# Kernel tuning notes

Hardware: AMD Instinct MI355X
Metric: run time of the kernel (lower is better)

The kernel has to match this reference:

```python
import jax, jax.numpy as jnp
import numpy as np

D_OUT = 32


def mlp(x, Ws, bs):
    # Ws: (L+1, d, d), bs: (L+1, d); relu after hidden layers, linear output
    h = x
    n = Ws.shape[0]
    for i in range(n - 1):
        h = jax.nn.relu(h @ Ws[i] + bs[i])
    return h @ Ws[n - 1] + bs[n - 1]


def causal_dot_product(Q, K, V, t1, t2):
    """out[:,:,i] = Q_i @ sum_{j: t2[j] <= t1[i]} K_j V_j^T.
    t2 is sorted (timestamps), so the cumulative outer-product state can be
    computed with a cumsum and gathered via searchsorted.
    Q: (1,1,T1,d); K,V: (1,1,T2,d); t1: (T1,); t2: (T2,).
    """
    outer = K[..., :, :, None] * V[..., :, None, :]      # (1,1,T2,d,d)
    S = jnp.cumsum(outer, axis=2)                        # prefix states
    idx = jnp.searchsorted(t2, t1, side='right') - 1     # (T1,)
    valid = idx >= 0
    Sg = S[:, :, jnp.maximum(idx, 0)]                    # (1,1,T1,d,d)
    out = jnp.einsum('bhid,bhide->bhie', Q, Sg)
    return jnp.where(valid[None, None, :, None], out, jnp.zeros((), out.dtype))


def _with_sorted_time(x, key):
    T = x.shape[2]
    t = jnp.sort(jax.random.uniform(key, (T,), dtype=jnp.float32)) * 100.0
    return x.at[0, 0, :, -1].set(t)


def setup_inputs() -> dict:
    key = jax.random.key(0)
    ks = jax.random.split(key, 16)
    d = 64
    Ts = [4096, 6144, 8192, 4096]
    mods = {}
    for i, T in enumerate(Ts):
        x = jax.random.normal(ks[i], (1, 1, T, d), dtype=jnp.float32)
        mods[f'm{i+1}'] = _with_sorted_time(x, ks[8 + i])
    scale = 1.0 / np.sqrt(d)
    WQ_w = jax.random.normal(ks[4], (3, d, d), dtype=jnp.float32) * scale
    WQ_b = jnp.zeros((3, d), dtype=jnp.float32)
    WK_w = jax.random.normal(ks[5], (4, 3, d, d), dtype=jnp.float32) * scale
    WK_b = jnp.zeros((4, 3, d), dtype=jnp.float32)
    return dict(m1=mods['m1'], m2=mods['m2'], m3=mods['m3'], m4=mods['m4'],
                WQ_w=WQ_w, WQ_b=WQ_b, WK_w=WK_w, WK_b=WK_b)


def reference(m1, m2, m3, m4, WQ_w, WQ_b, WK_w, WK_b):
    Q = mlp(m1, WQ_w, WQ_b)            # (1,1,T1,d)
    t1 = m1[0, 0, :, -1]               # (T1,)
    total = None
    for mi, X in enumerate([m1, m2, m3, m4]):
        K = mlp(X, WK_w[mi], WK_b[mi])
        V = X
        t2 = X[0, 0, :, -1]
        Z = causal_dot_product(Q, K, V, t1, t2)  # (1,1,T1,d)
        total = Z if total is None else total + Z
    # cat over dim=1 then sum(1) == sum of per-modality results, dim 1 dropped
    yhat = total.sum(axis=1)[..., :D_OUT]        # (1,T1,d_out)
    return yhat
```

## Files before the change

kernel.cpp:

```cpp
#include <hip/hip_runtime.h>


#define QB_OFF   0
#define KB_OFF   131072
#define SP_OFF   851968
#define TD_OFF   1581056

typedef __attribute__((ext_vector_type(8))) short short8;
typedef __attribute__((ext_vector_type(4))) float floatx4;

__device__ __forceinline__ unsigned short f2bf(float f) {
    union { float f; unsigned u; } v; v.f = f;
    unsigned r = v.u + 0x7fff + ((v.u >> 16) & 1);
    return (unsigned short)(r >> 16);
}
__device__ __forceinline__ float bf2f(unsigned short h) {
    union { unsigned u; float f; } v; v.u = ((unsigned)h) << 16;
    return v.f;
}

#define MFMA16(a,b,c) __builtin_amdgcn_mfma_f32_16x16x32_bf16((a),(b),(c),0,0,0)

__global__ __launch_bounds__(256) void k_fused(
    const float* __restrict__ x0, const float* __restrict__ x1,
    const float* __restrict__ x2, const float* __restrict__ x3,
    const float* __restrict__ wq_w, const float* __restrict__ wq_b,
    const float* __restrict__ wk_w, const float* __restrict__ wk_b,
    float* __restrict__ ws, float* __restrict__ out)
{
    __shared__ unsigned short H0[64*72];
    __shared__ unsigned short H1[64*72];
    __shared__ unsigned short Wt[3][64*72];
    __shared__ unsigned short KT[64*72];
    __shared__ unsigned short VT[32*72];

    const int tid = threadIdx.x;
    const int bid = blockIdx.x;

    int task, rb;
    if (bid < 64)       { task = 0; rb = bid; }
    else if (bid < 128) { task = 1; rb = bid - 64; }
    else if (bid < 224) { task = 2; rb = bid - 128; }
    else if (bid < 352) { task = 3; rb = bid - 224; }
    else                { task = 4; rb = bid - 352; }

    const float* Xs[4] = {x0, x1, x2, x3};
    const int rowoff[4] = {0, 4096, 10240, 18432};
    const int spoffc[4] = {0, 64, 160, 288};

    const float* X; const float* W; const float* Bv; int mm = -1;
    if (task == 0) { X = x0; W = wq_w; Bv = wq_b; }
    else {
        mm = task - 1;
        X = Xs[mm]; W = wk_w + mm*3*64*64; Bv = wk_b + mm*3*64;
    }

    const int row0 = rb * 64;

    {
        const float4* X4 = (const float4*)(X + (size_t)row0*64);
        #pragma unroll
        for (int k = 0; k < 4; ++k) {
            int idx = k*256 + tid;
            float4 v = X4[idx];
            int rr = idx >> 4, c4 = (idx & 15) * 4;
            ushort4 h;
            h.x = f2bf(v.x); h.y = f2bf(v.y); h.z = f2bf(v.z); h.w = f2bf(v.w);
            *(ushort4*)&H0[rr*72 + c4] = h;
        }
        const float4* W4 = (const float4*)W;
        #pragma unroll
        for (int k = 0; k < 12; ++k) {
            int idx = k*256 + tid;
            float4 v = W4[idx];
            int l = idx >> 10, rest = idx & 1023;
            int d = rest >> 4, c4 = (rest & 15) * 4;
            Wt[l][(c4+0)*72 + d] = f2bf(v.x);
            Wt[l][(c4+1)*72 + d] = f2bf(v.y);
            Wt[l][(c4+2)*72 + d] = f2bf(v.z);
            Wt[l][(c4+3)*72 + d] = f2bf(v.w);
        }
    }
    if (task == 0) {
        float4 z = make_float4(0.f, 0.f, 0.f, 0.f);
        ((float4*)out)[bid*512 + tid] = z;
        ((float4*)out)[bid*512 + 256 + tid] = z;
    }
    if (task > 0 && tid < 64)
        ws[TD_OFF + rowoff[mm] + row0 + tid] = X[(size_t)(row0 + tid)*64 + 63];
    __syncthreads();

    const int w    = tid >> 6;
    const int lane = tid & 63;
    const int lm   = lane & 15;
    const int q    = lane >> 4;
    const int col  = w*16 + lm;

    #pragma unroll 1
    for (int l = 0; l < 3; ++l) {
        const unsigned short* Hin  = (l & 1) ? H1 : H0;
        unsigned short*       Hout = (l & 1) ? H0 : H1;
        float bias = Bv[l*64 + col];
        short8 b0 = *(const short8*)&Wt[l][col*72 + q*8];
        short8 b1 = *(const short8*)&Wt[l][col*72 + 32 + q*8];
        #pragma unroll
        for (int mt = 0; mt < 4; ++mt) {
            floatx4 acc = {bias, bias, bias, bias};
            short8 a0 = *(const short8*)&Hin[(mt*16+lm)*72 + q*8];
            short8 a1 = *(const short8*)&Hin[(mt*16+lm)*72 + 32 + q*8];
            acc = MFMA16(a0, b0, acc);
            acc = MFMA16(a1, b1, acc);
            int r0 = mt*16 + q*4;
            #pragma unroll
            for (int r = 0; r < 4; ++r) {
                float f = acc[r];
                if (l < 2) f = fmaxf(f, 0.0f);
                unsigned short hb = f2bf(f);
                Hout[(r0+r)*72 + col] = hb;
                if (l == 2 && task > 0) KT[col*72 + r0 + r] = hb;
            }
        }
        __syncthreads();
    }

    {
        unsigned short* dst = (task == 0)
            ? (unsigned short*)(ws + QB_OFF)
            : (unsigned short*)(ws + KB_OFF) + (size_t)rowoff[mm]*64;
        #pragma unroll
        for (int k = 0; k < 4; ++k) {
            int idx = k*256 + tid;
            int rr = idx >> 4, c4 = (idx & 15) * 4;
            *(ushort4*)&dst[(size_t)(row0 + rr)*64 + c4] = *(ushort4*)&H1[rr*72 + c4];
        }
    }
    if (task == 0) return;

    {
        #pragma unroll
        for (int k = 0; k < 2; ++k) {
            int idx = k*256 + tid;
            int j = idx >> 3, e4 = (idx & 7) * 4;
            float4 v = *(const float4*)&X[(size_t)(row0 + j)*64 + e4];
            VT[(e4+0)*72 + j] = f2bf(v.x);
            VT[(e4+1)*72 + j] = f2bf(v.y);
            VT[(e4+2)*72 + j] = f2bf(v.z);
            VT[(e4+3)*72 + j] = f2bf(v.w);
        }
    }
    __syncthreads();

    {
        unsigned short* slotH = (unsigned short*)(ws + SP_OFF)
                              + (size_t)(spoffc[mm] + rb) * 2048;
        #pragma unroll
        for (int nt = 0; nt < 2; ++nt) {
            floatx4 acc = {0.f, 0.f, 0.f, 0.f};
            #pragma unroll
            for (int ks = 0; ks < 2; ++ks) {
                short8 aa = *(const short8*)&KT[col*72 + ks*32 + q*8];
                short8 bb = *(const short8*)&VT[(nt*16+lm)*72 + ks*32 + q*8];
                acc = MFMA16(aa, bb, acc);
            }
            #pragma unroll
            for (int r = 0; r < 4; ++r)
                slotH[(w*16 + q*4 + r)*32 + nt*16 + lm] = f2bf(acc[r]);
        }
    }
}

__global__ __launch_bounds__(256) void k_query(
    const float* __restrict__ x0, const float* __restrict__ x1,
    const float* __restrict__ x2, const float* __restrict__ x3,
    float* __restrict__ ws, float* __restrict__ out)
{
    __shared__ unsigned short qs[64*72];
    __shared__ unsigned short kc[64*72];
    __shared__ unsigned short vt[32*72];
    __shared__ unsigned short st[32*72];
    __shared__ unsigned short ps[64*72];
    __shared__ float tq[64];
    __shared__ float tcs[64];
    __shared__ int   SB[2];

    const int tid  = threadIdx.x;
    const int m    = blockIdx.x & 3;
    const int tile = (blockIdx.x >> 2) & 63;
    const int slot = blockIdx.x >> 8;
    const int i0   = tile * 64;

    const int w    = tid >> 6;
    const int lane = tid & 63;
    const int lm   = lane & 15;
    const int q    = lane >> 4;

    const float* Xs[4] = {x0, x1, x2, x3};
    const int rowoff[4] = {0, 4096, 10240, 18432};
    const int spoffc[4] = {0, 64, 160, 288};
    const int Tm[4]     = {4096, 6144, 8192, 4096};
    const float* X = Xs[m];

    const unsigned short* Qg  = (const unsigned short*)(ws + QB_OFF);
    const unsigned short* Kg  = (const unsigned short*)(ws + KB_OFF) + (size_t)rowoff[m]*64;
    const unsigned short* SPH = (const unsigned short*)(ws + SP_OFF);
    const float* td = ws + TD_OFF;

    #pragma unroll
    for (int k = 0; k < 4; ++k) {
        int idx = k*256 + tid;
        int rr = idx >> 4, c4 = (idx & 15) * 4;
        *(ushort4*)&qs[rr*72 + c4] = *(const ushort4*)&Qg[(size_t)(i0 + rr)*64 + c4];
    }
    if (tid < 64) tq[tid] = td[i0 + tid];

    if (w < 2) {
        float t = td[i0 + (w ? 63 : 0)];
        const float* t2 = td + rowoff[m];
        int lo = 0, hi = Tm[m];
        while (hi - lo > 64) {
            int step = (hi - lo + 63) >> 6;
            int pos = lo + lane*step;
            bool pred = (pos < hi) && (t2[pos] <= t);
            int c = __popcll(__ballot(pred));
            int nhi = (c < 64) ? (lo + c*step) : hi;
            if (nhi > hi) nhi = hi;
            if (c) lo = lo + (c-1)*step + 1;
            hi = nhi;
        }
        int pos = lo + lane;
        bool pred = (pos < hi) && (t2[pos] <= t);
        int c = __popcll(__ballot(pred));
        if (lane == 0) SB[w] = lo + c;
    }
    __syncthreads();

    const int c_lo = SB[0];
    const int c_hi = SB[1];
    const int B0   = c_lo >> 6;
    const int Bhi  = (c_hi + 63) >> 6;

    {
        float sacc[8] = {0.f,0.f,0.f,0.f,0.f,0.f,0.f,0.f};
        const unsigned short* sp0 = SPH + (size_t)spoffc[m]*2048 + tid*8;
        #pragma unroll 2
        for (int k = slot; k < B0; k += 2) {
            uint4 pv = *(const uint4*)(sp0 + (size_t)k*2048);
            sacc[0] += bf2f((unsigned short)(pv.x & 0xffffu));
            sacc[1] += bf2f((unsigned short)(pv.x >> 16));
            sacc[2] += bf2f((unsigned short)(pv.y & 0xffffu));
            sacc[3] += bf2f((unsigned short)(pv.y >> 16));
            sacc[4] += bf2f((unsigned short)(pv.z & 0xffffu));
            sacc[5] += bf2f((unsigned short)(pv.z >> 16));
            sacc[6] += bf2f((unsigned short)(pv.w & 0xffffu));
            sacc[7] += bf2f((unsigned short)(pv.w >> 16));
        }
        int d0 = (tid*8) >> 5, e0 = (tid*8) & 31;
        #pragma unroll
        for (int k = 0; k < 8; ++k)
            st[(e0+k)*72 + d0] = f2bf(sacc[k]);
    }
    __syncthreads();

    float t1v[16];
    #pragma unroll
    for (int mt = 0; mt < 4; ++mt)
        #pragma unroll
        for (int r = 0; r < 4; ++r)
            t1v[mt*4 + r] = tq[mt*16 + q*4 + r];

    short8 qa[4][2];
    #pragma unroll
    for (int mt = 0; mt < 4; ++mt) {
        qa[mt][0] = *(const short8*)&qs[(mt*16+lm)*72 + q*8];
        qa[mt][1] = *(const short8*)&qs[(mt*16+lm)*72 + 32 + q*8];
    }

    floatx4 accO[2];
    accO[0] = (floatx4){0.f, 0.f, 0.f, 0.f};
    accO[1] = (floatx4){0.f, 0.f, 0.f, 0.f};

    #pragma unroll
    for (int nt = 0; nt < 2; ++nt) {
        #pragma unroll
        for (int ks = 0; ks < 2; ++ks) {
            short8 b = *(const short8*)&st[(nt*16+lm)*72 + ks*32 + q*8];
            accO[nt] = MFMA16(qa[w][ks], b, accO[nt]);
        }
    }

    #pragma unroll 1
    for (int B = B0 + slot; B < Bhi; B += 2) {
        __syncthreads();
        #pragma unroll
        for (int k = 0; k < 4; ++k) {
            int idx = k*256 + tid;
            int j = idx >> 4, c4 = (idx & 15) * 4;
            *(ushort4*)&kc[j*72 + c4] = *(const ushort4*)&Kg[(size_t)(B*64 + j)*64 + c4];
        }
        #pragma unroll
        for (int k = 0; k < 2; ++k) {
            int idx = k*256 + tid;
            int j = idx >> 3, e4 = (idx & 7) * 4;
            float4 v = *(const float4*)&X[(size_t)(B*64 + j)*64 + e4];
            vt[(e4+0)*72 + j] = f2bf(v.x);
            vt[(e4+1)*72 + j] = f2bf(v.y);
            vt[(e4+2)*72 + j] = f2bf(v.z);
            vt[(e4+3)*72 + j] = f2bf(v.w);
        }
        if (tid < 64) tcs[tid] = td[rowoff[m] + B*64 + tid];
        __syncthreads();

        {
            short8 bk0 = *(const short8*)&kc[(w*16+lm)*72 + q*8];
            short8 bk1 = *(const short8*)&kc[(w*16+lm)*72 + 32 + q*8];
            float t2j = tcs[w*16 + lm];
            #pragma unroll
            for (int mt = 0; mt < 4; ++mt) {
                floatx4 f = {0.f, 0.f, 0.f, 0.f};
                f = MFMA16(qa[mt][0], bk0, f);
                f = MFMA16(qa[mt][1], bk1, f);
                #pragma unroll
                for (int r = 0; r < 4; ++r) {
                    float p = (t2j <= t1v[mt*4 + r]) ? f[r] : 0.0f;
                    ps[(mt*16 + q*4 + r)*72 + w*16 + lm] = f2bf(p);
                }
            }
        }
        __syncthreads();

        {
            short8 pa0 = *(const short8*)&ps[(w*16+lm)*72 + q*8];
            short8 pa1 = *(const short8*)&ps[(w*16+lm)*72 + 32 + q*8];
            #pragma unroll
            for (int nt = 0; nt < 2; ++nt) {
                short8 bv0 = *(const short8*)&vt[(nt*16+lm)*72 + q*8];
                short8 bv1 = *(const short8*)&vt[(nt*16+lm)*72 + 32 + q*8];
                accO[nt] = MFMA16(pa0, bv0, accO[nt]);
                accO[nt] = MFMA16(pa1, bv1, accO[nt]);
            }
        }
    }

    #pragma unroll
    for (int nt = 0; nt < 2; ++nt)
        #pragma unroll
        for (int r = 0; r < 4; ++r) {
            int i = w*16 + q*4 + r;
            int e = nt*16 + lm;
            atomicAdd(&out[(size_t)(i0 + i)*32 + e], accO[nt][r]);
        }
}

extern "C" void kernel_launch(void* const* d_in, const int* in_sizes, int n_in,
                              void* d_out, int out_size, void* d_ws, size_t ws_size,
                              hipStream_t stream) {
    const float* x0   = (const float*)d_in[0];
    const float* x1   = (const float*)d_in[1];
    const float* x2   = (const float*)d_in[2];
    const float* x3   = (const float*)d_in[3];
    const float* wq_w = (const float*)d_in[4];
    const float* wq_b = (const float*)d_in[5];
    const float* wk_w = (const float*)d_in[6];
    const float* wk_b = (const float*)d_in[7];
    float* ws  = (float*)d_ws;
    float* out = (float*)d_out;

    hipLaunchKernelGGL(k_fused, dim3(416), dim3(256), 0, stream,
                       x0, x1, x2, x3, wq_w, wq_b, wk_w, wk_b, ws, out);
    hipLaunchKernelGGL(k_query, dim3(512), dim3(256), 0, stream,
                       x0, x1, x2, x3, ws, out);
}
```

Before: 105.9 us.

## Precompute transposed bf16 V tiles in fused kernel and reuse in query kernel

The fused kernel now builds the transposed bf16 V tile from the X values already loaded for the MLP, instead of re-reading X from global memory. It also writes that tile to a new workspace region, so the query kernel loads ready-made bf16 V tiles with vector copies rather than re-reading fp32 X and transposing it. Global loads of X and W are batched up front, and the prefix-state reduction loop is unrolled to keep four loads in flight. The cost is extra workspace writes and more registers held for the batched loads.

```diff
diff --git a/kernel.cpp b/kernel.cpp
--- a/kernel.cpp
+++ b/kernel.cpp
@@ -4,6 +4,7 @@
 #define QB_OFF   0
 #define KB_OFF   131072
 #define SP_OFF   851968
+#define VB_OFF   1212416
 #define TD_OFF   1581056
 
 typedef __attribute__((ext_vector_type(8))) short short8;
@@ -59,26 +60,38 @@
 
     {
         const float4* X4 = (const float4*)(X + (size_t)row0*64);
+        float4 xv[4];
+        #pragma unroll
+        for (int k = 0; k < 4; ++k) xv[k] = X4[k*256 + tid];
+        const float4* W4 = (const float4*)W;
+        float4 wv[12];
+        #pragma unroll
+        for (int k = 0; k < 12; ++k) wv[k] = W4[k*256 + tid];
+
         #pragma unroll
         for (int k = 0; k < 4; ++k) {
             int idx = k*256 + tid;
-            float4 v = X4[idx];
             int rr = idx >> 4, c4 = (idx & 15) * 4;
             ushort4 h;
-            h.x = f2bf(v.x); h.y = f2bf(v.y); h.z = f2bf(v.z); h.w = f2bf(v.w);
+            h.x = f2bf(xv[k].x); h.y = f2bf(xv[k].y);
+            h.z = f2bf(xv[k].z); h.w = f2bf(xv[k].w);
             *(ushort4*)&H0[rr*72 + c4] = h;
-        }
-        const float4* W4 = (const float4*)W;
+            if (task > 0 && c4 < 32) {
+                VT[(c4+0)*72 + rr] = h.x;
+                VT[(c4+1)*72 + rr] = h.y;
+                VT[(c4+2)*72 + rr] = h.z;
+                VT[(c4+3)*72 + rr] = h.w;
+            }
+        }
         #pragma unroll
         for (int k = 0; k < 12; ++k) {
             int idx = k*256 + tid;
-            float4 v = W4[idx];
             int l = idx >> 10, rest = idx & 1023;
             int d = rest >> 4, c4 = (rest & 15) * 4;
-            Wt[l][(c4+0)*72 + d] = f2bf(v.x);
-            Wt[l][(c4+1)*72 + d] = f2bf(v.y);
-            Wt[l][(c4+2)*72 + d] = f2bf(v.z);
-            Wt[l][(c4+3)*72 + d] = f2bf(v.w);
+            Wt[l][(c4+0)*72 + d] = f2bf(wv[k].x);
+            Wt[l][(c4+1)*72 + d] = f2bf(wv[k].y);
+            Wt[l][(c4+2)*72 + d] = f2bf(wv[k].z);
+            Wt[l][(c4+3)*72 + d] = f2bf(wv[k].w);
         }
     }
     if (task == 0) {
@@ -89,6 +102,17 @@
     if (task > 0 && tid < 64)
         ws[TD_OFF + rowoff[mm] + row0 + tid] = X[(size_t)(row0 + tid)*64 + 63];
     __syncthreads();
+
+    if (task > 0) {
+        unsigned short* VBg = (unsigned short*)(ws + VB_OFF)
+                            + (size_t)(spoffc[mm] + rb) * 2048;
+        #pragma unroll
+        for (int k = 0; k < 2; ++k) {
+            int p = k*256 + tid;
+            int e = p >> 4, j4 = (p & 15) * 4;
+            *(ushort4*)&VBg[p*4] = *(ushort4*)&VT[e*72 + j4];
+        }
+    }
 
     const int w    = tid >> 6;
     const int lane = tid & 63;
@@ -137,20 +161,6 @@
     if (task == 0) return;
 
     {
-        #pragma unroll
-        for (int k = 0; k < 2; ++k) {
-            int idx = k*256 + tid;
-            int j = idx >> 3, e4 = (idx & 7) * 4;
-            float4 v = *(const float4*)&X[(size_t)(row0 + j)*64 + e4];
-            VT[(e4+0)*72 + j] = f2bf(v.x);
-            VT[(e4+1)*72 + j] = f2bf(v.y);
-            VT[(e4+2)*72 + j] = f2bf(v.z);
-            VT[(e4+3)*72 + j] = f2bf(v.w);
-        }
-    }
-    __syncthreads();
-
-    {
         unsigned short* slotH = (unsigned short*)(ws + SP_OFF)
                               + (size_t)(spoffc[mm] + rb) * 2048;
         #pragma unroll
@@ -170,8 +180,6 @@
 }
 
 __global__ __launch_bounds__(256) void k_query(
-    const float* __restrict__ x0, const float* __restrict__ x1,
-    const float* __restrict__ x2, const float* __restrict__ x3,
     float* __restrict__ ws, float* __restrict__ out)
 {
     __shared__ unsigned short qs[64*72];
@@ -194,15 +202,14 @@
     const int lm   = lane & 15;
     const int q    = lane >> 4;
 
-    const float* Xs[4] = {x0, x1, x2, x3};
     const int rowoff[4] = {0, 4096, 10240, 18432};
     const int spoffc[4] = {0, 64, 160, 288};
     const int Tm[4]     = {4096, 6144, 8192, 4096};
-    const float* X = Xs[m];
 
     const unsigned short* Qg  = (const unsigned short*)(ws + QB_OFF);
     const unsigned short* Kg  = (const unsigned short*)(ws + KB_OFF) + (size_t)rowoff[m]*64;
     const unsigned short* SPH = (const unsigned short*)(ws + SP_OFF);
+    const unsigned short* VBH = (const unsigned short*)(ws + VB_OFF);
     const float* td = ws + TD_OFF;
 
     #pragma unroll
@@ -242,22 +249,33 @@
     {
         float sacc[8] = {0.f,0.f,0.f,0.f,0.f,0.f,0.f,0.f};
         const unsigned short* sp0 = SPH + (size_t)spoffc[m]*2048 + tid*8;
-        #pragma unroll 2
-        for (int k = slot; k < B0; k += 2) {
-            uint4 pv = *(const uint4*)(sp0 + (size_t)k*2048);
-            sacc[0] += bf2f((unsigned short)(pv.x & 0xffffu));
-            sacc[1] += bf2f((unsigned short)(pv.x >> 16));
-            sacc[2] += bf2f((unsigned short)(pv.y & 0xffffu));
-            sacc[3] += bf2f((unsigned short)(pv.y >> 16));
-            sacc[4] += bf2f((unsigned short)(pv.z & 0xffffu));
-            sacc[5] += bf2f((unsigned short)(pv.z >> 16));
-            sacc[6] += bf2f((unsigned short)(pv.w & 0xffffu));
-            sacc[7] += bf2f((unsigned short)(pv.w >> 16));
-        }
+#define ACC8(pv) do { \
+            sacc[0] += bf2f((unsigned short)((pv).x & 0xffffu)); \
+            sacc[1] += bf2f((unsigned short)((pv).x >> 16)); \
+            sacc[2] += bf2f((unsigned short)((pv).y & 0xffffu)); \
+            sacc[3] += bf2f((unsigned short)((pv).y >> 16)); \
+            sacc[4] += bf2f((unsigned short)((pv).z & 0xffffu)); \
+            sacc[5] += bf2f((unsigned short)((pv).z >> 16)); \
+            sacc[6] += bf2f((unsigned short)((pv).w & 0xffffu)); \
+            sacc[7] += bf2f((unsigned short)((pv).w >> 16)); \
+        } while (0)
+        int k = slot;
+        for (; k + 6 < B0; k += 8) {
+            uint4 p0 = *(const uint4*)(sp0 + (size_t)(k  )*2048);
+            uint4 p1 = *(const uint4*)(sp0 + (size_t)(k+2)*2048);
+            uint4 p2 = *(const uint4*)(sp0 + (size_t)(k+4)*2048);
+            uint4 p3 = *(const uint4*)(sp0 + (size_t)(k+6)*2048);
+            ACC8(p0); ACC8(p1); ACC8(p2); ACC8(p3);
+        }
+        for (; k < B0; k += 2) {
+            uint4 p0 = *(const uint4*)(sp0 + (size_t)k*2048);
+            ACC8(p0);
+        }
+#undef ACC8
         int d0 = (tid*8) >> 5, e0 = (tid*8) & 31;
         #pragma unroll
-        for (int k = 0; k < 8; ++k)
-            st[(e0+k)*72 + d0] = f2bf(sacc[k]);
+        for (int k2 = 0; k2 < 8; ++k2)
+            st[(e0+k2)*72 + d0] = f2bf(sacc[k2]);
     }
     __syncthreads();
 
@@ -297,15 +315,14 @@
             int j = idx >> 4, c4 = (idx & 15) * 4;
             *(ushort4*)&kc[j*72 + c4] = *(const ushort4*)&Kg[(size_t)(B*64 + j)*64 + c4];
         }
-        #pragma unroll
-        for (int k = 0; k < 2; ++k) {
-            int idx = k*256 + tid;
-            int j = idx >> 3, e4 = (idx & 7) * 4;
-            float4 v = *(const float4*)&X[(size_t)(B*64 + j)*64 + e4];
-            vt[(e4+0)*72 + j] = f2bf(v.x);
-            vt[(e4+1)*72 + j] = f2bf(v.y);
-            vt[(e4+2)*72 + j] = f2bf(v.z);
-            vt[(e4+3)*72 + j] = f2bf(v.w);
+        {
+            const unsigned short* VBg = VBH + (size_t)(spoffc[m] + B)*2048;
+            #pragma unroll
+            for (int k = 0; k < 2; ++k) {
+                int p = k*256 + tid;
+                int e = p >> 4, j4 = (p & 15) * 4;
+                *(ushort4*)&vt[e*72 + j4] = *(const ushort4*)&VBg[p*4];
+            }
         }
         if (tid < 64) tcs[tid] = td[rowoff[m] + B*64 + tid];
         __syncthreads();
@@ -367,6 +384,5 @@
 
     hipLaunchKernelGGL(k_fused, dim3(416), dim3(256), 0, stream,
                        x0, x1, x2, x3, wq_w, wq_b, wk_w, wk_b, ws, out);
-    hipLaunchKernelGGL(k_query, dim3(512), dim3(256), 0, stream,
-                       x0, x1, x2, x3, ws, out);
-}
+    hipLaunchKernelGGL(k_query, dim3(512), dim3(256), 0, stream, ws, out);
+}
```

Result: faster. 98.61 us (median of 2 runs) (-6.8%).
